# Optimization experiments

Measured on AMD Instinct MI355X. Metric: run time of the kernel, lower is better.

Reference implementation:

```python
import jax, jax.numpy as jnp
import numpy as np

N_QUBITS = 4
BATCH = 262144

_CNOT = jnp.array([[1, 0, 0, 0],
                   [0, 1, 0, 0],
                   [0, 0, 0, 1],
                   [0, 0, 1, 0]], dtype=jnp.complex64).reshape(2, 2, 2, 2)


def _apply_1q(state, gate, wire):
    # state: (2,)*N_QUBITS, gate: (2,2). Contract gate into axis `wire`.
    state = jnp.tensordot(gate, state, axes=([1], [wire]))
    return jnp.moveaxis(state, 0, wire)


def _apply_cnot(state, ctrl, tgt):
    state = jnp.tensordot(_CNOT, state, axes=([2, 3], [ctrl, tgt]))
    return jnp.moveaxis(state, (0, 1), (ctrl, tgt))


def _circuit(x, w):
    # x: (N_QUBITS,) input angles, w: (N_QUBITS,) trainable angles
    state = jnp.zeros((2,) * N_QUBITS, jnp.complex64).at[(0,) * N_QUBITS].set(1.0)
    half_x = (x * 0.5).astype(jnp.complex64)
    half_w = (w * 0.5).astype(jnp.complex64)
    for i in range(N_QUBITS):
        c, s = jnp.cos(half_x[i]), jnp.sin(half_x[i])
        rx = jnp.array([[c, -1j * s], [-1j * s, c]])
        state = _apply_1q(state, rx, i)
        cy, sy = jnp.cos(half_w[i]), jnp.sin(half_w[i])
        ry = jnp.array([[cy, -sy], [sy, cy]])
        state = _apply_1q(state, ry, i)
    for i in range(N_QUBITS - 1):
        state = _apply_cnot(state, i, i + 1)
    probs = jnp.real(state * jnp.conj(state))  # (2,2,2,2)
    zs = []
    for i in range(N_QUBITS):
        other = tuple(a for a in range(N_QUBITS) if a != i)
        p = probs.sum(axis=other)  # (2,)
        zs.append(p[0] - p[1])  # <Z_i> = P(0) - P(1)
    return jnp.stack(zs).astype(jnp.float32)  # (N_QUBITS,)


def setup_inputs() -> dict:
    key = jax.random.key(0)
    kx, kw = jax.random.split(key)
    x = jax.random.normal(kx, (BATCH, N_QUBITS), dtype=jnp.float32)
    weights = 0.01 * jax.random.normal(kw, (N_QUBITS,), dtype=jnp.float32)
    return {"x": x, "weights": weights}


def reference(x, weights):
    # Batched state-vector simulation of the 4-qubit RX/RY/CNOT circuit.
    return jax.vmap(lambda xi: _circuit(xi, weights))(x)  # (BATCH, N_QUBITS)
```

## Files before the change

### kernel.cpp

```cpp
#include <hip/hip_runtime.h>


__global__ void __launch_bounds__(256)
QuantumLayer_56607668961323_kernel(const float4* __restrict__ x,
                                   const float* __restrict__ w,
                                   float4* __restrict__ out,
                                   int n) {
    int i = blockIdx.x * blockDim.x + threadIdx.x;
    if (i >= n) return;

    float cw0 = cosf(w[0]);
    float cw1 = cosf(w[1]);
    float cw2 = cosf(w[2]);
    float cw3 = cosf(w[3]);

    float4 xv = x[i];
    float z0 = cosf(xv.x) * cw0;
    float z1 = z0 * cosf(xv.y) * cw1;
    float z2 = z1 * cosf(xv.z) * cw2;
    float z3 = z2 * cosf(xv.w) * cw3;

    out[i] = make_float4(z0, z1, z2, z3);
}

extern "C" void kernel_launch(void* const* d_in, const int* in_sizes, int n_in,
                              void* d_out, int out_size, void* d_ws, size_t ws_size,
                              hipStream_t stream) {
    const float4* x = (const float4*)d_in[0];
    const float*  w = (const float*)d_in[1];
    float4* out = (float4*)d_out;

    int n = in_sizes[0] / 4;
    int block = 256;
    int grid = (n + block - 1) / block;
    QuantumLayer_56607668961323_kernel<<<grid, block, 0, stream>>>(x, w, out, n);
}
```

Before: 9.733 us.

## Use hardware cosine intrinsic and process two rows per thread

Replaces the accurate cosf library calls with the AMDGCN hardware cosine intrinsic, which takes its input in revolutions and needs a scale by 1/(2π). It also precomputes the cumulative weight-cosine products and has each thread handle two float4 rows, halving the grid. This removes the software range-reduction work and spreads per-thread overhead over more rows. The hardware cosine loses accuracy for large arguments. The inputs are normal samples, so arguments stay small.

```diff
diff --git a/kernel.cpp b/kernel.cpp
--- a/kernel.cpp
+++ b/kernel.cpp
@@ -1,26 +1,43 @@
 #include <hip/hip_runtime.h>
 
+
+#define INV_2PI 0.15915494309189535f
 
 __global__ void __launch_bounds__(256)
 QuantumLayer_56607668961323_kernel(const float4* __restrict__ x,
                                    const float* __restrict__ w,
                                    float4* __restrict__ out,
                                    int n) {
-    int i = blockIdx.x * blockDim.x + threadIdx.x;
-    if (i >= n) return;
+    int i = (blockIdx.x * blockDim.x + threadIdx.x) * 2;
 
-    float cw0 = cosf(w[0]);
-    float cw1 = cosf(w[1]);
-    float cw2 = cosf(w[2]);
-    float cw3 = cosf(w[3]);
+    float cw0 = __builtin_amdgcn_cosf(w[0] * INV_2PI);
+    float cw1 = cw0 * __builtin_amdgcn_cosf(w[1] * INV_2PI);
+    float cw2 = cw1 * __builtin_amdgcn_cosf(w[2] * INV_2PI);
+    float cw3 = cw2 * __builtin_amdgcn_cosf(w[3] * INV_2PI);
 
-    float4 xv = x[i];
-    float z0 = cosf(xv.x) * cw0;
-    float z1 = z0 * cosf(xv.y) * cw1;
-    float z2 = z1 * cosf(xv.z) * cw2;
-    float z3 = z2 * cosf(xv.w) * cw3;
+    if (i + 1 < n) {
+        float4 a = x[i];
+        float4 b = x[i + 1];
 
-    out[i] = make_float4(z0, z1, z2, z3);
+        float a0 = __builtin_amdgcn_cosf(a.x * INV_2PI);
+        float a1 = a0 * __builtin_amdgcn_cosf(a.y * INV_2PI);
+        float a2 = a1 * __builtin_amdgcn_cosf(a.z * INV_2PI);
+        float a3 = a2 * __builtin_amdgcn_cosf(a.w * INV_2PI);
+        out[i] = make_float4(a0 * cw0, a1 * cw1, a2 * cw2, a3 * cw3);
+
+        float b0 = __builtin_amdgcn_cosf(b.x * INV_2PI);
+        float b1 = b0 * __builtin_amdgcn_cosf(b.y * INV_2PI);
+        float b2 = b1 * __builtin_amdgcn_cosf(b.z * INV_2PI);
+        float b3 = b2 * __builtin_amdgcn_cosf(b.w * INV_2PI);
+        out[i + 1] = make_float4(b0 * cw0, b1 * cw1, b2 * cw2, b3 * cw3);
+    } else if (i < n) {
+        float4 a = x[i];
+        float a0 = __builtin_amdgcn_cosf(a.x * INV_2PI);
+        float a1 = a0 * __builtin_amdgcn_cosf(a.y * INV_2PI);
+        float a2 = a1 * __builtin_amdgcn_cosf(a.z * INV_2PI);
+        float a3 = a2 * __builtin_amdgcn_cosf(a.w * INV_2PI);
+        out[i] = make_float4(a0 * cw0, a1 * cw1, a2 * cw2, a3 * cw3);
+    }
 }
 
 extern "C" void kernel_launch(void* const* d_in, const int* in_sizes, int n_in,
@@ -32,6 +49,6 @@
 
     int n = in_sizes[0] / 4;
     int block = 256;
-    int grid = (n + block - 1) / block;
+    int grid = (n + block * 2 - 1) / (block * 2);
     QuantumLayer_56607668961323_kernel<<<grid, block, 0, stream>>>(x, w, out, n);
 }
```

After: 9.750 us. No clear change (+0.2%).
